# Performance work log

Hardware: AMD Instinct MI355X
Metric: run time of the kernel (lower is better)

Reference implementation:

```python
import jax, jax.numpy as jnp
import numpy as np

B = 8192
N_IN = 16 * 12 * 64  # 12288
H0, H1, H2 = 256, 32, 32
OUTPUT_SCALE = 300.0
WDL_SCALE = 200.0


def setup_inputs() -> dict:
    key = jax.random.key(0)
    ks = jax.random.split(key, 12)
    # In real NNUE these are ~30-hot binary vectors; math is identical for dense rand.
    white_features = (jax.random.uniform(ks[0], (B, N_IN)) < 0.0025).astype(jnp.float32)
    black_features = (jax.random.uniform(ks[1], (B, N_IN)) < 0.0025).astype(jnp.float32)
    side = jax.random.randint(ks[2], (B,), 0, 2).astype(bool)
    ft_std = np.sqrt(2.0 / (22 + H1))
    ft_w = jax.random.normal(ks[3], (H0, N_IN)) * ft_std
    ft_b = jnp.zeros((H0,))
    def xavier(k, fan_out, fan_in):
        std = np.sqrt(2.0 / (fan_in + fan_out))
        return jax.random.normal(k, (fan_out, fan_in)) * std
    l1_w = xavier(ks[4], H1, 2 * H0)
    l1_b = jnp.zeros((H1,))
    l2_w = xavier(ks[5], H2, H1)
    l2_b = jnp.zeros((H2,))
    l3_w = xavier(ks[6], 1, H2)
    l3_b = jnp.zeros((1,))
    return {"white_features": white_features, "black_features": black_features,
            "side": side, "ft_w": ft_w, "ft_b": ft_b, "l1_w": l1_w, "l1_b": l1_b,
            "l2_w": l2_w, "l2_b": l2_b, "l3_w": l3_w, "l3_b": l3_b}


def reference(white_features, black_features, side, ft_w, ft_b,
              l1_w, l1_b, l2_w, l2_b, l3_w, l3_b):
    w = white_features @ ft_w.T + ft_b  # [B, H0]
    b = black_features @ ft_w.T + ft_b  # [B, H0]
    s = side[:, None]  # [B, 1] bool
    # side-to-move first: white -> [w, b], black -> [b, w]
    acc = jnp.where(s, jnp.concatenate([w, b], axis=1),
                    jnp.concatenate([b, w], axis=1))  # [B, 2*H0]
    o0 = jnp.clip(acc, 0.0, 1.0)
    o1 = jnp.clip(o0 @ l1_w.T + l1_b, 0.0, 1.0)
    o2 = jnp.clip(o1 @ l2_w.T + l2_b, 0.0, 1.0)
    o3 = (o2 @ l3_w.T + l3_b) * OUTPUT_SCALE  # [B, 1]
    return jax.nn.sigmoid(o3 / WDL_SCALE)
```

## Files before the change

kernel.cpp:

```cpp
#include <hip/hip_runtime.h>
#include <math.h>


#define NIN   12288
#define NF4   3072
#define NDW   768
#define FPT   12
#define H0    256
#define MAXF  192

__global__ __launch_bounds__(256) void transpose_ftw(const float* __restrict__ src,
                                                     float* __restrict__ dst) {
    __shared__ float tile[32][33];
    const int jb = blockIdx.x * 32;
    const int hb = blockIdx.y * 32;
    const int tx = threadIdx.x;
    const int ty = threadIdx.y;
#pragma unroll
    for (int r = 0; r < 32; r += 8)
        tile[ty + r][tx] = src[(size_t)(hb + ty + r) * NIN + jb + tx];
    __syncthreads();
#pragma unroll
    for (int r = 0; r < 32; r += 8)
        dst[(size_t)(jb + ty + r) * H0 + hb + tx] = tile[tx][ty + r];
}

__device__ __forceinline__ unsigned char mask4(uint4 u) {
    return (unsigned char)((u.x ? 1u : 0u) | (u.y ? 2u : 0u) |
                           (u.z ? 4u : 0u) | (u.w ? 8u : 0u));
}

__global__ __launch_bounds__(256) void scan_kernel(const uint4* __restrict__ white,
                                                   const uint4* __restrict__ black,
                                                   unsigned char* __restrict__ wbm,
                                                   unsigned char* __restrict__ bbm,
                                                   int total)
{
    const int stride = gridDim.x * 256;
    int i = blockIdx.x * 256 + threadIdx.x;
    for (; i + 3 * stride < total; i += 4 * stride) {
        const uint4 w0 = white[i];
        const uint4 w1 = white[i + stride];
        const uint4 w2 = white[i + 2 * stride];
        const uint4 w3 = white[i + 3 * stride];
        const uint4 b0 = black[i];
        const uint4 b1 = black[i + stride];
        const uint4 b2 = black[i + 2 * stride];
        const uint4 b3 = black[i + 3 * stride];
        wbm[i]              = mask4(w0);
        wbm[i + stride]     = mask4(w1);
        wbm[i + 2 * stride] = mask4(w2);
        wbm[i + 3 * stride] = mask4(w3);
        bbm[i]              = mask4(b0);
        bbm[i + stride]     = mask4(b1);
        bbm[i + 2 * stride] = mask4(b2);
        bbm[i + 3 * stride] = mask4(b3);
    }
    for (; i < total; i += stride) {
        wbm[i] = mask4(white[i]);
        bbm[i] = mask4(black[i]);
    }
}

__global__ __launch_bounds__(256) void gather_kernel(
    const int* __restrict__ side,
    const float* __restrict__ ftw,
    const float* __restrict__ ft_b,
    const float* __restrict__ l1_w,
    const float* __restrict__ l1_b,
    const float* __restrict__ l2_w,
    const float* __restrict__ l2_b,
    const float* __restrict__ l3_w,
    const float* __restrict__ l3_b,
    const unsigned char* __restrict__ wbm,
    const unsigned char* __restrict__ bbm,
    float* __restrict__ out)
{
    __shared__ int w_list[MAXF];
    __shared__ int b_list[MAXF];
    __shared__ int w_cnt, b_cnt;
    __shared__ float sh_o0[512] __attribute__((aligned(16)));
    __shared__ float sh_o1[32];
    __shared__ float sh_o2[32];

    const int s   = blockIdx.x;
    const int tid = threadIdx.x;

    if (tid == 0) { w_cnt = 0; b_cnt = 0; }
    __syncthreads();

    const unsigned* wrow = (const unsigned*)(wbm + (size_t)s * NF4);
    const unsigned* brow = (const unsigned*)(bbm + (size_t)s * NF4);
#pragma unroll
    for (int q = 0; q < 3; ++q) {
        const int d = q * 256 + tid;
        unsigned v = wrow[d];
        while (v) {
            const int bpos = __ffs(v) - 1;
            const int j = ((d * 4 + (bpos >> 3)) << 2) + (bpos & 7);
            const int p = atomicAdd(&w_cnt, 1);
            if (p < MAXF) w_list[p] = j;
            v &= v - 1;
        }
        unsigned vb = brow[d];
        while (vb) {
            const int bpos = __ffs(vb) - 1;
            const int j = ((d * 4 + (bpos >> 3)) << 2) + (bpos & 7);
            const int p = atomicAdd(&b_cnt, 1);
            if (p < MAXF) b_list[p] = j;
            vb &= vb - 1;
        }
    }
    __syncthreads();

    const int wn = min(w_cnt, MAXF);
    const int bn = min(b_cnt, MAXF);

    const float bias = ft_b[tid];
    const float* col = ftw + tid;
    float wacc = bias;
    float bacc = bias;
    {
        int k = 0;
        for (; k + 8 <= wn; k += 8) {
            const float f0 = col[(size_t)w_list[k]     * H0];
            const float f1 = col[(size_t)w_list[k + 1] * H0];
            const float f2 = col[(size_t)w_list[k + 2] * H0];
            const float f3 = col[(size_t)w_list[k + 3] * H0];
            const float f4 = col[(size_t)w_list[k + 4] * H0];
            const float f5 = col[(size_t)w_list[k + 5] * H0];
            const float f6 = col[(size_t)w_list[k + 6] * H0];
            const float f7 = col[(size_t)w_list[k + 7] * H0];
            wacc += ((f0 + f1) + (f2 + f3)) + ((f4 + f5) + (f6 + f7));
        }
        for (; k < wn; ++k) wacc += col[(size_t)w_list[k] * H0];
        k = 0;
        for (; k + 8 <= bn; k += 8) {
            const float f0 = col[(size_t)b_list[k]     * H0];
            const float f1 = col[(size_t)b_list[k + 1] * H0];
            const float f2 = col[(size_t)b_list[k + 2] * H0];
            const float f3 = col[(size_t)b_list[k + 3] * H0];
            const float f4 = col[(size_t)b_list[k + 4] * H0];
            const float f5 = col[(size_t)b_list[k + 5] * H0];
            const float f6 = col[(size_t)b_list[k + 6] * H0];
            const float f7 = col[(size_t)b_list[k + 7] * H0];
            bacc += ((f0 + f1) + (f2 + f3)) + ((f4 + f5) + (f6 + f7));
        }
        for (; k < bn; ++k) bacc += col[(size_t)b_list[k] * H0];
    }
    const float ow = fminf(fmaxf(wacc, 0.f), 1.f);
    const float ob = fminf(fmaxf(bacc, 0.f), 1.f);
    const bool sd = (side[s] != 0);
    sh_o0[tid]       = sd ? ow : ob;
    sh_o0[256 + tid] = sd ? ob : ow;
    __syncthreads();

    {
        const int o = tid >> 3;
        const int p = tid & 7;
        const float4* wp = (const float4*)(l1_w + (o * 512 + p * 64));
        const float4* xp = (const float4*)(sh_o0 + p * 64);
        float sum = 0.f;
#pragma unroll
        for (int i = 0; i < 16; ++i) {
            const int v = (2 * p + i) & 15;
            float4 w4 = wp[v];
            float4 x4 = xp[v];
            sum += w4.x * x4.x + w4.y * x4.y + w4.z * x4.z + w4.w * x4.w;
        }
        sum += __shfl_down(sum, 4, 8);
        sum += __shfl_down(sum, 2, 8);
        sum += __shfl_down(sum, 1, 8);
        if (p == 0) sh_o1[o] = fminf(fmaxf(sum + l1_b[o], 0.f), 1.f);
    }
    __syncthreads();

    if (tid < 32) {
        float sum = 0.f;
#pragma unroll
        for (int k = 0; k < 32; ++k) sum += l2_w[tid * 32 + k] * sh_o1[k];
        sh_o2[tid] = fminf(fmaxf(sum + l2_b[tid], 0.f), 1.f);
    }
    __syncthreads();

    if (tid < 32) {
        float p = l3_w[tid] * sh_o2[tid];
        p += __shfl_down(p, 16, 32);
        p += __shfl_down(p, 8, 32);
        p += __shfl_down(p, 4, 32);
        p += __shfl_down(p, 2, 32);
        p += __shfl_down(p, 1, 32);
        if (tid == 0) {
            const float o3  = (p + l3_b[0]) * 300.0f;
            out[s] = 1.0f / (1.0f + expf(-o3 / 200.0f));
        }
    }
}

template <bool TRANSPOSED>
__global__ __launch_bounds__(256) void nnue_kernel(
    const float* __restrict__ white, const float* __restrict__ black,
    const int* __restrict__ side, const float* __restrict__ ftw,
    const float* __restrict__ ft_b, const float* __restrict__ l1_w,
    const float* __restrict__ l1_b, const float* __restrict__ l2_w,
    const float* __restrict__ l2_b, const float* __restrict__ l3_w,
    const float* __restrict__ l3_b, float* __restrict__ out)
{
    __shared__ int w_list[MAXF];
    __shared__ int b_list[MAXF];
    __shared__ int w_cnt, b_cnt;
    __shared__ float sh_o0[512] __attribute__((aligned(16)));
    __shared__ float sh_o1[32];
    __shared__ float sh_o2[32];
    const int s = blockIdx.x, tid = threadIdx.x;
    if (tid == 0) { w_cnt = 0; b_cnt = 0; }
    __syncthreads();
    const uint4* wrow = (const uint4*)(white + (size_t)s * NIN);
    const uint4* brow = (const uint4*)(black + (size_t)s * NIN);
#pragma unroll
    for (int i = 0; i < FPT; ++i) {
        const int v = i * 256 + tid;
        uint4 u = wrow[v];
        if (u.x | u.y | u.z | u.w) {
            if (u.x) { int p = atomicAdd(&w_cnt, 1); if (p < MAXF) w_list[p] = v * 4 + 0; }
            if (u.y) { int p = atomicAdd(&w_cnt, 1); if (p < MAXF) w_list[p] = v * 4 + 1; }
            if (u.z) { int p = atomicAdd(&w_cnt, 1); if (p < MAXF) w_list[p] = v * 4 + 2; }
            if (u.w) { int p = atomicAdd(&w_cnt, 1); if (p < MAXF) w_list[p] = v * 4 + 3; }
        }
        uint4 b = brow[v];
        if (b.x | b.y | b.z | b.w) {
            if (b.x) { int p = atomicAdd(&b_cnt, 1); if (p < MAXF) b_list[p] = v * 4 + 0; }
            if (b.y) { int p = atomicAdd(&b_cnt, 1); if (p < MAXF) b_list[p] = v * 4 + 1; }
            if (b.z) { int p = atomicAdd(&b_cnt, 1); if (p < MAXF) b_list[p] = v * 4 + 2; }
            if (b.w) { int p = atomicAdd(&b_cnt, 1); if (p < MAXF) b_list[p] = v * 4 + 3; }
        }
    }
    __syncthreads();
    const int wn = min(w_cnt, MAXF), bn = min(b_cnt, MAXF);
    const float bias = ft_b[tid];
    float wacc = bias, bacc = bias;
    for (int k = 0; k < wn; ++k) {
        const int j = w_list[k];
        wacc += TRANSPOSED ? ftw[(size_t)j * H0 + tid] : ftw[(size_t)tid * NIN + j];
    }
    for (int k = 0; k < bn; ++k) {
        const int j = b_list[k];
        bacc += TRANSPOSED ? ftw[(size_t)j * H0 + tid] : ftw[(size_t)tid * NIN + j];
    }
    const float ow = fminf(fmaxf(wacc, 0.f), 1.f);
    const float ob = fminf(fmaxf(bacc, 0.f), 1.f);
    const bool sd = (side[s] != 0);
    sh_o0[tid] = sd ? ow : ob;
    sh_o0[256 + tid] = sd ? ob : ow;
    __syncthreads();
    {
        const int o = tid >> 3, p = tid & 7;
        const float4* wp = (const float4*)(l1_w + (o * 512 + p * 64));
        const float4* xp = (const float4*)(sh_o0 + p * 64);
        float sum = 0.f;
#pragma unroll
        for (int i = 0; i < 16; ++i) {
            const int v = (2 * p + i) & 15;
            float4 w4 = wp[v]; float4 x4 = xp[v];
            sum += w4.x * x4.x + w4.y * x4.y + w4.z * x4.z + w4.w * x4.w;
        }
        sum += __shfl_down(sum, 4, 8);
        sum += __shfl_down(sum, 2, 8);
        sum += __shfl_down(sum, 1, 8);
        if (p == 0) sh_o1[o] = fminf(fmaxf(sum + l1_b[o], 0.f), 1.f);
    }
    __syncthreads();
    if (tid < 32) {
        float sum = 0.f;
#pragma unroll
        for (int k = 0; k < 32; ++k) sum += l2_w[tid * 32 + k] * sh_o1[k];
        sh_o2[tid] = fminf(fmaxf(sum + l2_b[tid], 0.f), 1.f);
    }
    __syncthreads();
    if (tid < 32) {
        float p = l3_w[tid] * sh_o2[tid];
        p += __shfl_down(p, 16, 32);
        p += __shfl_down(p, 8, 32);
        p += __shfl_down(p, 4, 32);
        p += __shfl_down(p, 2, 32);
        p += __shfl_down(p, 1, 32);
        if (tid == 0) {
            const float o3 = (p + l3_b[0]) * 300.0f;
            out[s] = 1.0f / (1.0f + expf(-o3 / 200.0f));
        }
    }
}

extern "C" void kernel_launch(void* const* d_in, const int* in_sizes, int n_in,
                              void* d_out, int out_size, void* d_ws, size_t ws_size,
                              hipStream_t stream) {
    const float* white = (const float*)d_in[0];
    const float* black = (const float*)d_in[1];
    const int*   side  = (const int*)d_in[2];
    const float* ft_w  = (const float*)d_in[3];
    const float* ft_b  = (const float*)d_in[4];
    const float* l1_w  = (const float*)d_in[5];
    const float* l1_b  = (const float*)d_in[6];
    const float* l2_w  = (const float*)d_in[7];
    const float* l2_b  = (const float*)d_in[8];
    const float* l3_w  = (const float*)d_in[9];
    const float* l3_b  = (const float*)d_in[10];
    float*       out   = (float*)d_out;

    const int B = in_sizes[2];
    const size_t t_bytes  = (size_t)NIN * H0 * 4;
    const size_t bm_bytes = (size_t)B * NF4;
    const size_t need     = t_bytes + 2 * bm_bytes;

    if (ws_size >= need) {
        float*         ftw_t = (float*)d_ws;
        unsigned char* wbm   = (unsigned char*)d_ws + t_bytes;
        unsigned char* bbm   = wbm + bm_bytes;
        const int total = B * NF4;

        hipLaunchKernelGGL(transpose_ftw, dim3(NIN / 32, H0 / 32), dim3(32, 8), 0, stream,
                           ft_w, ftw_t);
        hipLaunchKernelGGL(scan_kernel, dim3(2048), dim3(256), 0, stream,
                           (const uint4*)white, (const uint4*)black, wbm, bbm, total);
        hipLaunchKernelGGL(gather_kernel, dim3(B), dim3(256), 0, stream,
                           side, ftw_t, ft_b, l1_w, l1_b, l2_w, l2_b, l3_w, l3_b,
                           wbm, bbm, out);
    } else if (ws_size >= t_bytes) {
        float* ftw_t = (float*)d_ws;
        hipLaunchKernelGGL(transpose_ftw, dim3(NIN / 32, H0 / 32), dim3(32, 8), 0, stream,
                           ft_w, ftw_t);
        hipLaunchKernelGGL((nnue_kernel<true>), dim3(B), dim3(256), 0, stream,
                           white, black, side, ftw_t, ft_b, l1_w, l1_b, l2_w, l2_b, l3_w, l3_b, out);
    } else {
        hipLaunchKernelGGL((nnue_kernel<false>), dim3(B), dim3(256), 0, stream,
                           white, black, side, ft_w, ft_b, l1_w, l1_b, l2_w, l2_b, l3_w, l3_b, out);
    }
}
```

Before: 944.5 us.

## Store transposed feature weights as bf16 and split gather threads by perspective

The transposed feature-transformer table is now rounded to bf16 and packed so each thread gathers two hidden units per load. Half the block accumulates the white perspective and the other half the black perspective, halving gather bytes. The bitmask scan kernel is restructured to one-shot blocks, each issuing 16 independent vector loads. The change trades fp32 accumulation inputs for bf16-rounded weights, which adds rounding error, and drops the transposed-fallback path.

```diff
diff --git a/kernel.cpp b/kernel.cpp
--- a/kernel.cpp
+++ b/kernel.cpp
@@ -4,13 +4,19 @@
 
 #define NIN   12288
 #define NF4   3072
-#define NDW   768
 #define FPT   12
 #define H0    256
 #define MAXF  192
 
-__global__ __launch_bounds__(256) void transpose_ftw(const float* __restrict__ src,
-                                                     float* __restrict__ dst) {
+__device__ __forceinline__ unsigned char mask4(uint4 u) {
+    return (unsigned char)((u.x ? 1u : 0u) | (u.y ? 2u : 0u) |
+                           (u.z ? 4u : 0u) | (u.w ? 8u : 0u));
+}
+__device__ __forceinline__ float bflo(unsigned u) { return __uint_as_float(u << 16); }
+__device__ __forceinline__ float bfhi(unsigned u) { return __uint_as_float(u & 0xFFFF0000u); }
+
+__global__ __launch_bounds__(256) void transpose_ftw_bf16(const float* __restrict__ src,
+                                                          unsigned short* __restrict__ dst) {
     __shared__ float tile[32][33];
     const int jb = blockIdx.x * 32;
     const int hb = blockIdx.y * 32;
@@ -21,50 +27,42 @@
         tile[ty + r][tx] = src[(size_t)(hb + ty + r) * NIN + jb + tx];
     __syncthreads();
 #pragma unroll
-    for (int r = 0; r < 32; r += 8)
-        dst[(size_t)(jb + ty + r) * H0 + hb + tx] = tile[tx][ty + r];
-}
-
-__device__ __forceinline__ unsigned char mask4(uint4 u) {
-    return (unsigned char)((u.x ? 1u : 0u) | (u.y ? 2u : 0u) |
-                           (u.z ? 4u : 0u) | (u.w ? 8u : 0u));
-}
-
-__global__ __launch_bounds__(256) void scan_kernel(const uint4* __restrict__ white,
-                                                   const uint4* __restrict__ black,
-                                                   unsigned char* __restrict__ wbm,
-                                                   unsigned char* __restrict__ bbm,
-                                                   int total)
+    for (int r = 0; r < 32; r += 8) {
+        const unsigned u = __float_as_uint(tile[tx][ty + r]);
+        const unsigned short h = (unsigned short)((u + 0x7FFFu + ((u >> 16) & 1u)) >> 16);
+        dst[(size_t)(jb + ty + r) * H0 + hb + tx] = h;
+    }
+}
+
+__global__ __launch_bounds__(256, 4) void scan_kernel(const uint4* __restrict__ white,
+                                                      const uint4* __restrict__ black,
+                                                      unsigned char* __restrict__ wbm,
+                                                      unsigned char* __restrict__ bbm,
+                                                      int total)
 {
-    const int stride = gridDim.x * 256;
-    int i = blockIdx.x * 256 + threadIdx.x;
-    for (; i + 3 * stride < total; i += 4 * stride) {
-        const uint4 w0 = white[i];
-        const uint4 w1 = white[i + stride];
-        const uint4 w2 = white[i + 2 * stride];
-        const uint4 w3 = white[i + 3 * stride];
-        const uint4 b0 = black[i];
-        const uint4 b1 = black[i + stride];
-        const uint4 b2 = black[i + 2 * stride];
-        const uint4 b3 = black[i + 3 * stride];
-        wbm[i]              = mask4(w0);
-        wbm[i + stride]     = mask4(w1);
-        wbm[i + 2 * stride] = mask4(w2);
-        wbm[i + 3 * stride] = mask4(w3);
-        bbm[i]              = mask4(b0);
-        bbm[i + stride]     = mask4(b1);
-        bbm[i + 2 * stride] = mask4(b2);
-        bbm[i + 3 * stride] = mask4(b3);
-    }
-    for (; i < total; i += stride) {
-        wbm[i] = mask4(white[i]);
-        bbm[i] = mask4(black[i]);
+    const int i0 = blockIdx.x * 2048 + threadIdx.x;
+    if (i0 + 7 * 256 < total) {
+        uint4 w[8], b[8];
+#pragma unroll
+        for (int k = 0; k < 8; ++k) w[k] = white[i0 + k * 256];
+#pragma unroll
+        for (int k = 0; k < 8; ++k) b[k] = black[i0 + k * 256];
+#pragma unroll
+        for (int k = 0; k < 8; ++k) wbm[i0 + k * 256] = mask4(w[k]);
+#pragma unroll
+        for (int k = 0; k < 8; ++k) bbm[i0 + k * 256] = mask4(b[k]);
+    } else {
+#pragma unroll
+        for (int k = 0; k < 8; ++k) {
+            const int i = i0 + k * 256;
+            if (i < total) { wbm[i] = mask4(white[i]); bbm[i] = mask4(black[i]); }
+        }
     }
 }
 
 __global__ __launch_bounds__(256) void gather_kernel(
     const int* __restrict__ side,
-    const float* __restrict__ ftw,
+    const unsigned* __restrict__ tab,
     const float* __restrict__ ft_b,
     const float* __restrict__ l1_w,
     const float* __restrict__ l1_b,
@@ -116,43 +114,42 @@
     const int wn = min(w_cnt, MAXF);
     const int bn = min(b_cnt, MAXF);
 
-    const float bias = ft_b[tid];
-    const float* col = ftw + tid;
-    float wacc = bias;
-    float bacc = bias;
+    const int  h       = tid & 127;
+    const bool isWhite = (tid < 128);
+    const int* lst     = isWhite ? w_list : b_list;
+    const int  n       = isWhite ? wn : bn;
+    const unsigned* colp = tab + h;
+
+    float accx = ft_b[2 * h];
+    float accy = ft_b[2 * h + 1];
     {
         int k = 0;
-        for (; k + 8 <= wn; k += 8) {
-            const float f0 = col[(size_t)w_list[k]     * H0];
-            const float f1 = col[(size_t)w_list[k + 1] * H0];
-            const float f2 = col[(size_t)w_list[k + 2] * H0];
-            const float f3 = col[(size_t)w_list[k + 3] * H0];
-            const float f4 = col[(size_t)w_list[k + 4] * H0];
-            const float f5 = col[(size_t)w_list[k + 5] * H0];
-            const float f6 = col[(size_t)w_list[k + 6] * H0];
-            const float f7 = col[(size_t)w_list[k + 7] * H0];
-            wacc += ((f0 + f1) + (f2 + f3)) + ((f4 + f5) + (f6 + f7));
-        }
-        for (; k < wn; ++k) wacc += col[(size_t)w_list[k] * H0];
-        k = 0;
-        for (; k + 8 <= bn; k += 8) {
-            const float f0 = col[(size_t)b_list[k]     * H0];
-            const float f1 = col[(size_t)b_list[k + 1] * H0];
-            const float f2 = col[(size_t)b_list[k + 2] * H0];
-            const float f3 = col[(size_t)b_list[k + 3] * H0];
-            const float f4 = col[(size_t)b_list[k + 4] * H0];
-            const float f5 = col[(size_t)b_list[k + 5] * H0];
-            const float f6 = col[(size_t)b_list[k + 6] * H0];
-            const float f7 = col[(size_t)b_list[k + 7] * H0];
-            bacc += ((f0 + f1) + (f2 + f3)) + ((f4 + f5) + (f6 + f7));
-        }
-        for (; k < bn; ++k) bacc += col[(size_t)b_list[k] * H0];
-    }
-    const float ow = fminf(fmaxf(wacc, 0.f), 1.f);
-    const float ob = fminf(fmaxf(bacc, 0.f), 1.f);
+        for (; k + 8 <= n; k += 8) {
+            const unsigned u0 = colp[(size_t)lst[k]     * 128];
+            const unsigned u1 = colp[(size_t)lst[k + 1] * 128];
+            const unsigned u2 = colp[(size_t)lst[k + 2] * 128];
+            const unsigned u3 = colp[(size_t)lst[k + 3] * 128];
+            const unsigned u4 = colp[(size_t)lst[k + 4] * 128];
+            const unsigned u5 = colp[(size_t)lst[k + 5] * 128];
+            const unsigned u6 = colp[(size_t)lst[k + 6] * 128];
+            const unsigned u7 = colp[(size_t)lst[k + 7] * 128];
+            accx += ((bflo(u0) + bflo(u1)) + (bflo(u2) + bflo(u3))) +
+                    ((bflo(u4) + bflo(u5)) + (bflo(u6) + bflo(u7)));
+            accy += ((bfhi(u0) + bfhi(u1)) + (bfhi(u2) + bfhi(u3))) +
+                    ((bfhi(u4) + bfhi(u5)) + (bfhi(u6) + bfhi(u7)));
+        }
+        for (; k < n; ++k) {
+            const unsigned u = colp[(size_t)lst[k] * 128];
+            accx += bflo(u);
+            accy += bfhi(u);
+        }
+    }
+    const float cx = fminf(fmaxf(accx, 0.f), 1.f);
+    const float cy = fminf(fmaxf(accy, 0.f), 1.f);
     const bool sd = (side[s] != 0);
-    sh_o0[tid]       = sd ? ow : ob;
-    sh_o0[256 + tid] = sd ? ob : ow;
+    const int base = (isWhite == sd) ? 0 : 256;
+    sh_o0[base + 2 * h]     = cx;
+    sh_o0[base + 2 * h + 1] = cy;
     __syncthreads();
 
     {
@@ -191,13 +188,12 @@
         p += __shfl_down(p, 2, 32);
         p += __shfl_down(p, 1, 32);
         if (tid == 0) {
-            const float o3  = (p + l3_b[0]) * 300.0f;
+            const float o3 = (p + l3_b[0]) * 300.0f;
             out[s] = 1.0f / (1.0f + expf(-o3 / 200.0f));
         }
     }
 }
 
-template <bool TRANSPOSED>
 __global__ __launch_bounds__(256) void nnue_kernel(
     const float* __restrict__ white, const float* __restrict__ black,
     const int* __restrict__ side, const float* __restrict__ ftw,
@@ -239,14 +235,8 @@
     const int wn = min(w_cnt, MAXF), bn = min(b_cnt, MAXF);
     const float bias = ft_b[tid];
     float wacc = bias, bacc = bias;
-    for (int k = 0; k < wn; ++k) {
-        const int j = w_list[k];
-        wacc += TRANSPOSED ? ftw[(size_t)j * H0 + tid] : ftw[(size_t)tid * NIN + j];
-    }
-    for (int k = 0; k < bn; ++k) {
-        const int j = b_list[k];
-        bacc += TRANSPOSED ? ftw[(size_t)j * H0 + tid] : ftw[(size_t)tid * NIN + j];
-    }
+    for (int k = 0; k < wn; ++k) wacc += ftw[(size_t)tid * NIN + w_list[k]];
+    for (int k = 0; k < bn; ++k) bacc += ftw[(size_t)tid * NIN + b_list[k]];
     const float ow = fminf(fmaxf(wacc, 0.f), 1.f);
     const float ob = fminf(fmaxf(bacc, 0.f), 1.f);
     const bool sd = (side[s] != 0);
@@ -308,31 +298,26 @@
     float*       out   = (float*)d_out;
 
     const int B = in_sizes[2];
-    const size_t t_bytes  = (size_t)NIN * H0 * 4;
+    const size_t t_bytes  = (size_t)NIN * H0 * 2;
     const size_t bm_bytes = (size_t)B * NF4;
     const size_t need     = t_bytes + 2 * bm_bytes;
 
     if (ws_size >= need) {
-        float*         ftw_t = (float*)d_ws;
-        unsigned char* wbm   = (unsigned char*)d_ws + t_bytes;
-        unsigned char* bbm   = wbm + bm_bytes;
+        unsigned short* ftw_t = (unsigned short*)d_ws;
+        unsigned char*  wbm   = (unsigned char*)d_ws + t_bytes;
+        unsigned char*  bbm   = wbm + bm_bytes;
         const int total = B * NF4;
 
-        hipLaunchKernelGGL(transpose_ftw, dim3(NIN / 32, H0 / 32), dim3(32, 8), 0, stream,
+        hipLaunchKernelGGL(transpose_ftw_bf16, dim3(NIN / 32, H0 / 32), dim3(32, 8), 0, stream,
                            ft_w, ftw_t);
-        hipLaunchKernelGGL(scan_kernel, dim3(2048), dim3(256), 0, stream,
+        hipLaunchKernelGGL(scan_kernel, dim3((total + 2047) / 2048), dim3(256), 0, stream,
                            (const uint4*)white, (const uint4*)black, wbm, bbm, total);
         hipLaunchKernelGGL(gather_kernel, dim3(B), dim3(256), 0, stream,
-                           side, ftw_t, ft_b, l1_w, l1_b, l2_w, l2_b, l3_w, l3_b,
-                           wbm, bbm, out);
-    } else if (ws_size >= t_bytes) {
-        float* ftw_t = (float*)d_ws;
-        hipLaunchKernelGGL(transpose_ftw, dim3(NIN / 32, H0 / 32), dim3(32, 8), 0, stream,
-                           ft_w, ftw_t);
-        hipLaunchKernelGGL((nnue_kernel<true>), dim3(B), dim3(256), 0, stream,
-                           white, black, side, ftw_t, ft_b, l1_w, l1_b, l2_w, l2_b, l3_w, l3_b, out);
+                           side, (const unsigned*)ftw_t, ft_b, l1_w, l1_b, l2_w, l2_b,
+                           l3_w, l3_b, wbm, bbm, out);
     } else {
-        hipLaunchKernelGGL((nnue_kernel<false>), dim3(B), dim3(256), 0, stream,
-                           white, black, side, ft_w, ft_b, l1_w, l1_b, l2_w, l2_b, l3_w, l3_b, out);
-    }
-}
+        hipLaunchKernelGGL(nnue_kernel, dim3(B), dim3(256), 0, stream,
+                           white, black, side, ft_w, ft_b, l1_w, l1_b, l2_w, l2_b,
+                           l3_w, l3_b, out);
+    }
+}
```

Measured after the change: 883.8 us. 6.4% less time.
